# Kernel tuning notes

Measured on AMD Instinct MI355X. Metric: run time of the kernel, lower is better.

Reference implementation:

```python
import jax, jax.numpy as jnp
import numpy as np

G, N, F_IN, H, C = 128, 512, 128, 128, 10
LAMB = 1.0
NEG_SLOPE = 0.2
P_EDGE = 32.0 / N  # avg degree ~32


def setup_inputs() -> dict:
    key = jax.random.key(0)
    ks = jax.random.split(key, 12)
    x = jax.random.normal(ks[0], (G, N, F_IN), dtype=jnp.float32)
    # symmetric 0/1 adjacency without self loops (per-graph dense block)
    a = (jax.random.uniform(ks[1], (G, N, N)) < P_EDGE).astype(jnp.float32)
    adj = jnp.maximum(a, jnp.swapaxes(a, 1, 2)) * (1.0 - jnp.eye(N, dtype=jnp.float32))

    def lin(k, fi, fo):
        return (jax.random.normal(k, (fi, fo), dtype=jnp.float32) / np.float32(np.sqrt(fi)))

    return {
        "x": x, "adj": adj,
        "W1": lin(ks[2], F_IN, H), "b1": jnp.zeros((H,), jnp.float32),
        "W2": lin(ks[3], H, H), "b2": jnp.zeros((H,), jnp.float32),
        "W3": lin(ks[4], H, H), "b3": jnp.zeros((H,), jnp.float32),
        "att1_s": 0.1 * jax.random.normal(ks[5], (H,), dtype=jnp.float32),
        "att1_d": 0.1 * jax.random.normal(ks[6], (H,), dtype=jnp.float32),
        "att2_s": 0.1 * jax.random.normal(ks[7], (H,), dtype=jnp.float32),
        "att2_d": 0.1 * jax.random.normal(ks[8], (H,), dtype=jnp.float32),
        "Wl1": lin(ks[9], 2 * H, H), "bl1": jnp.zeros((H,), jnp.float32),
        "Wl2": lin(ks[10], H, H // 2), "bl2": jnp.zeros((H // 2,), jnp.float32),
        "Wl3": lin(ks[11], H // 2, C), "bl3": jnp.zeros((C,), jnp.float32),
    }


def gcn(x, adj, W, b):
    # GCNConv: D^{-1/2} (A + I) D^{-1/2} X W + b  (self-loop weight 1, edge weights in adj)
    deg = adj.sum(-1) + 1.0                              # [G, n]
    dinv = jax.lax.rsqrt(deg)
    xw = x @ W                                           # [G, n, H]
    agg = jnp.einsum('gij,gjf->gif', adj, dinv[..., None] * xw)
    return dinv[..., None] * agg + (dinv * dinv)[..., None] * xw + b


def info_score(x, adj):
    # HGP-SL node information score: row-wise L1 norm of (I - D^{-1} A) X
    deg = jnp.maximum(adj.sum(-1), 1.0)
    agg = jnp.einsum('gij,gjf->gif', adj, x) / deg[..., None]
    return jnp.sum(jnp.abs(x - agg), axis=-1)            # [G, n]


def hgpsl_pool(x, adj, att_s, att_d, k):
    # top-k node selection by information score, then structure learning:
    # dense (sample=False) path: e_ij = leaky_relu(att.[x_i||x_j]) + lamb*A_ij, softmax over j
    s = info_score(x, adj)
    _, idx = jax.lax.top_k(s, k)                         # [G, k]
    xk = jnp.take_along_axis(x, idx[..., None], axis=1)  # [G, k, H]
    g = jnp.arange(x.shape[0])[:, None, None]
    ak = adj[g, idx[:, :, None], idx[:, None, :]]        # induced adjacency [G, k, k]
    e = jax.nn.leaky_relu((xk @ att_s)[:, :, None] + (xk @ att_d)[:, None, :], NEG_SLOPE)
    attn = jax.nn.softmax(e + LAMB * ak, axis=-1)        # new learned edge weights
    return xk, attn


def readout(x):
    # gmp || gap over nodes
    return jnp.concatenate([x.max(axis=1), x.mean(axis=1)], axis=-1)


def reference(x, adj, W1, b1, W2, b2, W3, b3, att1_s, att1_d, att2_s, att2_d,
              Wl1, bl1, Wl2, bl2, Wl3, bl3):
    h = jax.nn.relu(gcn(x, adj, W1, b1))
    h, a1 = hgpsl_pool(h, adj, att1_s, att1_d, N // 2)
    x1 = readout(h)
    h = jax.nn.relu(gcn(h, a1, W2, b2))
    h, a2 = hgpsl_pool(h, a1, att2_s, att2_d, N // 4)
    x2 = readout(h)
    h = jax.nn.relu(gcn(h, a2, W3, b3))
    x3 = readout(h)
    z = jax.nn.relu(x1) + jax.nn.relu(x2) + jax.nn.relu(x3)
    z = jax.nn.relu(z @ Wl1 + bl1)
    z = jax.nn.relu(z @ Wl2 + bl2)
    return jax.nn.softmax(z @ Wl3 + bl3, axis=-1)
```

## Files before the change

kernel.cpp:

```cpp
#include <hip/hip_runtime.h>

#define Gg   128
#define N1   512
#define FH   128
#define K1   256
#define K2   128

typedef __bf16 bf16x8 __attribute__((ext_vector_type(8)));
typedef float  floatx4 __attribute__((ext_vector_type(4)));

__device__ inline float wredsum(float v) {
#pragma unroll
    for (int o = 32; o; o >>= 1) v += __shfl_xor(v, o, 64);
    return v;
}
__device__ inline float wredmax(float v) {
#pragma unroll
    for (int o = 32; o; o >>= 1) v = fmaxf(v, __shfl_xor(v, o, 64));
    return v;
}
__device__ inline unsigned short bf_rne(float x) {
    unsigned u = __float_as_uint(x);
    return (unsigned short)((u + 0x7fffu + ((u >> 16) & 1u)) >> 16);
}
__device__ __forceinline__ void gll16(const void* gsrc, void* lds) {
    __builtin_amdgcn_global_load_lds(
        (const __attribute__((address_space(1))) unsigned int*)gsrc,
        (__attribute__((address_space(3))) unsigned int*)lds, 16, 0, 0);
}

__global__ __launch_bounds__(256) void k_prep(const float* __restrict__ adj,
        unsigned short* __restrict__ adjbf,
        float* __restrict__ dinv_gcn, float* __restrict__ dinv_info) {
    int wave = threadIdx.x >> 6, lane = threadIdx.x & 63;
    long long row = (long long)blockIdx.x * 4 + wave;
    const float* ar = adj + row * N1;
    float s = 0.f;
    unsigned short ub[8] __attribute__((aligned(16)));
#pragma unroll
    for (int c = 0; c < 2; ++c) {
        float4 v = *(const float4*)(ar + lane * 8 + c * 4);
        s += (v.x + v.y) + (v.z + v.w);
        ub[c * 4 + 0] = (unsigned short)(__float_as_uint(v.x) >> 16);
        ub[c * 4 + 1] = (unsigned short)(__float_as_uint(v.y) >> 16);
        ub[c * 4 + 2] = (unsigned short)(__float_as_uint(v.z) >> 16);
        ub[c * 4 + 3] = (unsigned short)(__float_as_uint(v.w) >> 16);
    }
    *(uint4*)(adjbf + row * N1 + lane * 8) = *(const uint4*)ub;
    s = wredsum(s);
    if (lane == 0) {
        dinv_gcn[row]  = rsqrtf(s + 1.0f);
        dinv_info[row] = 1.0f / fmaxf(s, 1.0f);
    }
}

__global__ __launch_bounds__(256) void k_tsplit(const float* __restrict__ feat,
        unsigned short* __restrict__ Thi, unsigned short* __restrict__ Tmid,
        unsigned short* __restrict__ Tlo) {
    __shared__ float tile[64 * 65];
    int b = blockIdx.x;
    int g = b >> 4, rb = (b >> 1) & 7, cb = b & 1;
    int t = threadIdx.x;
    {
        int r0 = t >> 4, c4 = t & 15;
#pragma unroll
        for (int i = 0; i < 4; ++i) {
            int r = r0 + i * 16;
            float4 v = *(const float4*)(feat + ((long long)g * 512 + rb * 64 + r) * 128 + cb * 64 + c4 * 4);
            tile[r * 65 + c4 * 4 + 0] = v.x;
            tile[r * 65 + c4 * 4 + 1] = v.y;
            tile[r * 65 + c4 * 4 + 2] = v.z;
            tile[r * 65 + c4 * 4 + 3] = v.w;
        }
    }
    __syncthreads();
    int tf = t >> 2, chunk = t & 3;
    unsigned short hbuf[16] __attribute__((aligned(16)));
    unsigned short mbuf[16] __attribute__((aligned(16)));
    unsigned short lbuf[16] __attribute__((aligned(16)));
#pragma unroll
    for (int i = 0; i < 16; ++i) {
        int m = chunk * 16 + i;
        float v = tile[m * 65 + tf];
        unsigned short h = bf_rne(v);
        float fh = __uint_as_float((unsigned)h << 16);
        float r1 = v - fh;
        unsigned short md = bf_rne(r1);
        float fm = __uint_as_float((unsigned)md << 16);
        float r2 = r1 - fm;
        unsigned short lo = bf_rne(r2);
        hbuf[i] = h; mbuf[i] = md; lbuf[i] = lo;
    }
    int sxz = (tf >> 1) & 3;
    int c0 = (chunk & 1) * 2;
    int p0 = (c0 ^ sxz) * 8, p1 = ((c0 + 1) ^ sxz) * 8;
    long long obase = (long long)g * 65536 + (rb * 2 + (chunk >> 1)) * 4096
                    + (cb * 64 + tf) * 32;
    *(uint4*)(Thi + obase + p0)  = *(const uint4*)&hbuf[0];
    *(uint4*)(Thi + obase + p1)  = *(const uint4*)&hbuf[8];
    *(uint4*)(Tmid + obase + p0) = *(const uint4*)&mbuf[0];
    *(uint4*)(Tmid + obase + p1) = *(const uint4*)&mbuf[8];
    *(uint4*)(Tlo + obase + p0)  = *(const uint4*)&lbuf[0];
    *(uint4*)(Tlo + obase + p1)  = *(const uint4*)&lbuf[8];
}

template<int EPI>
__global__ __launch_bounds__(256) void k_aggmm(const unsigned short* __restrict__ adjbf,
        const unsigned short* __restrict__ Bhi, const unsigned short* __restrict__ Bmid,
        const unsigned short* __restrict__ Blo,
        const float* __restrict__ dvec, const float* __restrict__ hx,
        const float* __restrict__ bias, float* __restrict__ outH, float* __restrict__ outS) {
    __shared__ unsigned short Al[2][4096];
    __shared__ unsigned short Blin[2][3][4096];
    __shared__ float sred[2][128];
    int b = blockIdx.x;
    int g  = (b & 7) + ((b >> 5) << 3);
    int rb = (b >> 3) & 3;
    int tid = threadIdx.x;
    int w = tid >> 6, lane = tid & 63;
    int wm = w >> 1, wn = w & 1;
    int ln = lane & 15, quad = lane >> 4;
    int aoff = ((quad ^ ((lane >> 1) & 3)) << 4);
    floatx4 acc[4][4];
#pragma unroll
    for (int i = 0; i < 4; ++i)
#pragma unroll
        for (int j = 0; j < 4; ++j) { floatx4 z = {0.f, 0.f, 0.f, 0.f}; acc[i][j] = z; }

    const char* bsrc0 = (const char*)(Bhi  + (long long)g * 65536);
    const char* bsrc1 = (const char*)(Bmid + (long long)g * 65536);
    const char* bsrc2 = (const char*)(Blo  + (long long)g * 65536);
    int r1 = w * 32 + (lane >> 2);
    int c1 = (lane & 3) ^ ((r1 >> 1) & 3);
    int r2 = r1 + 16;
    int c2 = (lane & 3) ^ ((r2 >> 1) & 3);
    const unsigned short* abase = adjbf + ((long long)g * 512 + rb * 128) * 512;
    const unsigned short* asrc1 = abase + (long long)r1 * 512 + c1 * 8;
    const unsigned short* asrc2 = abase + (long long)r2 * 512 + c2 * 8;

#define STAGE(bi, kkv) do {                                                   \
        char* aldst = (char*)&Al[bi][0] + w * 2048;                           \
        gll16(asrc1 + (kkv), aldst);                                          \
        gll16(asrc2 + (kkv), aldst + 1024);                                   \
        long long soff = (long long)((kkv) >> 5) * 8192 + (w * 2048) + (lane << 4); \
        char* l0 = (char*)&Blin[bi][0][0] + w * 2048;                         \
        char* l1 = (char*)&Blin[bi][1][0] + w * 2048;                         \
        char* l2 = (char*)&Blin[bi][2][0] + w * 2048;                         \
        gll16(bsrc0 + soff,        l0);                                       \
        gll16(bsrc0 + soff + 1024, l0 + 1024);                                \
        gll16(bsrc1 + soff,        l1);                                       \
        gll16(bsrc1 + soff + 1024, l1 + 1024);                                \
        gll16(bsrc2 + soff,        l2);                                       \
        gll16(bsrc2 + soff + 1024, l2 + 1024);                                \
    } while (0)

    STAGE(0, 0);
    for (int kk = 0; kk < 512; kk += 32) {
        int cur = (kk >> 5) & 1;
        if (kk + 32 < 512) {
            STAGE(cur ^ 1, kk + 32);
            asm volatile("s_waitcnt vmcnt(8)" ::: "memory");
        } else {
            asm volatile("s_waitcnt vmcnt(0)" ::: "memory");
        }
        __builtin_amdgcn_sched_barrier(0);
        __builtin_amdgcn_s_barrier();
        bf16x8 af[4];
#pragma unroll
        for (int tm = 0; tm < 4; ++tm)
            af[tm] = *(const bf16x8*)((const char*)&Al[cur][0] + (wm * 64 + tm * 16 + ln) * 64 + aoff);
#pragma unroll
        for (int s = 0; s < 3; ++s) {
#pragma unroll
            for (int tn = 0; tn < 4; ++tn) {
                bf16x8 bfr = *(const bf16x8*)((const char*)&Blin[cur][s][0]
                                              + (wn * 64 + tn * 16 + ln) * 64 + aoff);
#pragma unroll
                for (int tm = 0; tm < 4; ++tm)
                    acc[tm][tn] = __builtin_amdgcn_mfma_f32_16x16x32_bf16(af[tm], bfr, acc[tm][tn], 0, 0, 0);
            }
        }
        __builtin_amdgcn_sched_barrier(0);
        __builtin_amdgcn_s_barrier();
    }
#undef STAGE
    long long rowbase = (long long)g * 512 + rb * 128;
    if (EPI == 0) {
#pragma unroll
        for (int tm = 0; tm < 4; ++tm)
#pragma unroll
        for (int r = 0; r < 4; ++r) {
            int ml = wm * 64 + tm * 16 + quad * 4 + r;
            long long grow = rowbase + ml;
            float di = dvec[grow];
#pragma unroll
            for (int tn = 0; tn < 4; ++tn) {
                int nc = wn * 64 + tn * 16 + ln;
                float hv = hx[grow * 128 + nc];
                float o = fmaxf(fmaf(di, acc[tm][tn][r] + hv, bias[nc]), 0.f);
                outH[grow * 128 + nc] = o;
            }
        }
    } else {
#pragma unroll
        for (int tm = 0; tm < 4; ++tm)
#pragma unroll
        for (int r = 0; r < 4; ++r) {
            int ml = wm * 64 + tm * 16 + quad * 4 + r;
            long long grow = rowbase + ml;
            float di = dvec[grow];
            float v = 0.f;
#pragma unroll
            for (int tn = 0; tn < 4; ++tn) {
                int nc = wn * 64 + tn * 16 + ln;
                float hv = hx[grow * 128 + nc];
                v += fabsf(hv - acc[tm][tn][r] * di);
            }
            v += __shfl_xor(v, 1); v += __shfl_xor(v, 2);
            v += __shfl_xor(v, 4); v += __shfl_xor(v, 8);
            if (ln == 0) sred[wn][ml] = v;
        }
        __syncthreads();
        if (tid < 128) outS[rowbase + tid] = sred[0][tid] + sred[1][tid];
    }
}

__global__ __launch_bounds__(256) void k_gemm_rw(const float* __restrict__ A,
        const float* __restrict__ W, float* __restrict__ C,
        const float* __restrict__ rs) {
    __shared__ float Al[64][68];
    __shared__ float Wl[64][132];
    long long row0 = (long long)blockIdx.x * 64;
    int tid = threadIdx.x, tr = tid >> 4, tc = tid & 15;
    float acc[4][8] = {};
    for (int ch = 0; ch < 2; ++ch) {
        for (int p = tid; p < 1024; p += 256) {
            int r = p >> 4, c4 = p & 15;
            *(float4*)&Al[r][c4 * 4] = *(const float4*)(A + (row0 + r) * 128 + ch * 64 + c4 * 4);
        }
        for (int p = tid; p < 2048; p += 256) {
            int r = p >> 5, c4 = p & 31;
            *(float4*)&Wl[r][c4 * 4] = *(const float4*)(W + (ch * 64 + r) * 128 + c4 * 4);
        }
        __syncthreads();
        for (int k = 0; k < 64; ++k) {
            float4 w0 = *(const float4*)&Wl[k][tc * 8];
            float4 w1 = *(const float4*)&Wl[k][tc * 8 + 4];
            float w[8] = {w0.x, w0.y, w0.z, w0.w, w1.x, w1.y, w1.z, w1.w};
#pragma unroll
            for (int i = 0; i < 4; ++i) {
                float a = Al[tr * 4 + i][k];
#pragma unroll
                for (int j = 0; j < 8; ++j) acc[i][j] = fmaf(a, w[j], acc[i][j]);
            }
        }
        __syncthreads();
    }
#pragma unroll
    for (int i = 0; i < 4; ++i) {
        long long r = row0 + tr * 4 + i;
        float sc = rs ? rs[r] : 1.0f;
        *(float4*)(C + r * 128 + tc * 8)     = make_float4(sc * acc[i][0], sc * acc[i][1], sc * acc[i][2], sc * acc[i][3]);
        *(float4*)(C + r * 128 + tc * 8 + 4) = make_float4(sc * acc[i][4], sc * acc[i][5], sc * acc[i][6], sc * acc[i][7]);
    }
}

template<int NT, int KSEL>
__global__ __launch_bounds__(256) void k_topk(const float* __restrict__ s, int* __restrict__ idx) {
    __shared__ unsigned long long keys[NT];
    int g = blockIdx.x;
    const float* sg = s + g * NT;
    for (int t = threadIdx.x; t < NT; t += 256) {
        unsigned int b = __float_as_uint(sg[t]);
        unsigned int ord = (b & 0x80000000u) ? ~b : (b | 0x80000000u);
        keys[t] = ((unsigned long long)(~ord) << 32) | (unsigned int)t;
    }
    __syncthreads();
    for (int k = 2; k <= NT; k <<= 1) {
        for (int j = k >> 1; j > 0; j >>= 1) {
            for (int i = threadIdx.x; i < NT; i += 256) {
                int l = i ^ j;
                if (l > i) {
                    bool dir = ((i & k) == 0);
                    unsigned long long a = keys[i], b2 = keys[l];
                    bool sw = dir ? (a > b2) : (a < b2);
                    if (sw) { keys[i] = b2; keys[l] = a; }
                }
            }
            __syncthreads();
        }
    }
    for (int t = threadIdx.x; t < KSEL; t += 256)
        idx[g * KSEL + t] = (int)(keys[t] & 0xffffffffu);
}

template<int KK>
__global__ __launch_bounds__(256) void k_gather(const float* __restrict__ h, int srcN,
        const int* __restrict__ idx, const float* __restrict__ atts, const float* __restrict__ attd,
        float* __restrict__ xk, float* __restrict__ as_, float* __restrict__ ad_) {
    int wave = threadIdx.x >> 6, lane = threadIdx.x & 63;
    int r = blockIdx.x * 4 + wave;
    int g = r / KK;
    int j = idx[r];
    float2 v = *(const float2*)(h + ((long long)g * srcN + j) * 128 + lane * 2);
    *(float2*)(xk + (long long)r * 128 + lane * 2) = v;
    float2 sv = *(const float2*)(atts + lane * 2);
    float2 dv = *(const float2*)(attd + lane * 2);
    float ps = v.x * sv.x + v.y * sv.y;
    float pd = v.x * dv.x + v.y * dv.y;
    ps = wredsum(ps); pd = wredsum(pd);
    if (lane == 0) { as_[r] = ps; ad_[r] = pd; }
}

template<int KK, int SRCN>
__global__ __launch_bounds__(256) void k_attn(const float* __restrict__ adjSrc,
        const int* __restrict__ idx, const float* __restrict__ as_, const float* __restrict__ ad_,
        float* __restrict__ attn, float* __restrict__ dgo, float* __restrict__ dio) {
    constexpr int E = KK / 64;
    __shared__ int   idxL[KK];
    __shared__ float adL[KK];
    __shared__ float rowL[4][SRCN];
    int bpg = KK / 4;
    int g = blockIdx.x / bpg;
    int wave = threadIdx.x >> 6, lane = threadIdx.x & 63;
    int i = (blockIdx.x % bpg) * 4 + wave;
    for (int t = threadIdx.x; t < KK; t += 256) { idxL[t] = idx[g * KK + t]; adL[t] = ad_[g * KK + t]; }
    __syncthreads();
    int ri = idxL[i];
    const float* arow = adjSrc + ((long long)g * SRCN + ri) * SRCN;
    for (int c = lane; c < SRCN; c += 64) rowL[wave][c] = arow[c];
    float asi = as_[g * KK + i];
    float vals[E];
    float m = -1e30f;
#pragma unroll
    for (int e = 0; e < E; ++e) {
        int j = e * 64 + lane;
        float x = asi + adL[j];
        x = (x >= 0.f) ? x : 0.2f * x;
        x += rowL[wave][idxL[j]];
        vals[e] = x; m = fmaxf(m, x);
    }
    m = wredmax(m);
    float S = 0.f;
#pragma unroll
    for (int e = 0; e < E; ++e) { vals[e] = expf(vals[e] - m); S += vals[e]; }
    S = wredsum(S);
    float inv = 1.f / S, rs = 0.f;
    float* orow = attn + ((long long)g * KK + i) * KK;
#pragma unroll
    for (int e = 0; e < E; ++e) { float p = vals[e] * inv; rs += p; orow[e * 64 + lane] = p; }
    rs = wredsum(rs);
    if (lane == 0) { dgo[g * KK + i] = rsqrtf(rs + 1.f); dio[g * KK + i] = 1.f / fmaxf(rs, 1.f); }
}

template<int KK>
__global__ __launch_bounds__(128) void k_readout(const float* __restrict__ xk, float* __restrict__ xo) {
    int g = blockIdx.x, f = threadIdx.x;
    const float* p = xk + (long long)g * KK * 128 + f;
    float m = -1e30f, s = 0.f;
    for (int r = 0; r < KK; ++r) { float v = p[r * 128]; m = fmaxf(m, v); s += v; }
    xo[g * 256 + f] = m;
    xo[g * 256 + 128 + f] = s * (1.0f / KK);
}

template<int KK, bool SCALEY, int EPI>
__global__ __launch_bounds__(256) void k_agg(const float* __restrict__ A, const float* __restrict__ Y,
        const float* __restrict__ dg, const float* __restrict__ di_,
        const float* __restrict__ bias, const float* __restrict__ hx,
        float* __restrict__ outH, float* __restrict__ outS) {
    __shared__ float Al[64][68];
    __shared__ float Yl[64][132];
    __shared__ float red[64][17];
    constexpr int RB = KK / 64;
    int g = blockIdx.x / RB;
    int rb = blockIdx.x % RB;
    const float* Ag = A + (long long)g * KK * KK;
    const float* Yg = Y + (long long)g * KK * 128;
    int tid = threadIdx.x, tr = tid >> 4, tc = tid & 15;
    float acc[4][8] = {};
    for (int ch = 0; ch < KK / 64; ++ch) {
        for (int p = tid; p < 1024; p += 256) {
            int r = p >> 4, c4 = p & 15;
            *(float4*)&Al[r][c4 * 4] = *(const float4*)(Ag + (rb * 64 + r) * KK + ch * 64 + c4 * 4);
        }
        for (int p = tid; p < 2048; p += 256) {
            int r = p >> 5, c4 = p & 31;
            float4 v = *(const float4*)(Yg + (ch * 64 + r) * 128 + c4 * 4);
            if (SCALEY) { float sc = dg[g * KK + ch * 64 + r]; v.x *= sc; v.y *= sc; v.z *= sc; v.w *= sc; }
            *(float4*)&Yl[r][c4 * 4] = v;
        }
        __syncthreads();
        for (int k = 0; k < 64; ++k) {
            float4 w0 = *(const float4*)&Yl[k][tc * 8];
            float4 w1 = *(const float4*)&Yl[k][tc * 8 + 4];
            float w[8] = {w0.x, w0.y, w0.z, w0.w, w1.x, w1.y, w1.z, w1.w};
#pragma unroll
            for (int i = 0; i < 4; ++i) {
                float a = Al[tr * 4 + i][k];
#pragma unroll
                for (int j = 0; j < 8; ++j) acc[i][j] = fmaf(a, w[j], acc[i][j]);
            }
        }
        __syncthreads();
    }
    int i0 = rb * 64 + tr * 4;
    if (EPI == 0) {
#pragma unroll
        for (int i = 0; i < 4; ++i) {
            long long gi = (long long)g * KK + i0 + i;
            float d = dg[gi], dd = d * d;
            float4 x0 = *(const float4*)(hx + gi * 128 + tc * 8);
            float4 x1 = *(const float4*)(hx + gi * 128 + tc * 8 + 4);
            float4 b0 = *(const float4*)(bias + tc * 8);
            float4 b1 = *(const float4*)(bias + tc * 8 + 4);
            float4 o0, o1;
            o0.x = fmaxf(fmaf(d, acc[i][0], fmaf(dd, x0.x, b0.x)), 0.f);
            o0.y = fmaxf(fmaf(d, acc[i][1], fmaf(dd, x0.y, b0.y)), 0.f);
            o0.z = fmaxf(fmaf(d, acc[i][2], fmaf(dd, x0.z, b0.z)), 0.f);
            o0.w = fmaxf(fmaf(d, acc[i][3], fmaf(dd, x0.w, b0.w)), 0.f);
            o1.x = fmaxf(fmaf(d, acc[i][4], fmaf(dd, x1.x, b1.x)), 0.f);
            o1.y = fmaxf(fmaf(d, acc[i][5], fmaf(dd, x1.y, b1.y)), 0.f);
            o1.z = fmaxf(fmaf(d, acc[i][6], fmaf(dd, x1.z, b1.z)), 0.f);
            o1.w = fmaxf(fmaf(d, acc[i][7], fmaf(dd, x1.w, b1.w)), 0.f);
            *(float4*)(outH + gi * 128 + tc * 8)     = o0;
            *(float4*)(outH + gi * 128 + tc * 8 + 4) = o1;
        }
    } else {
#pragma unroll
        for (int i = 0; i < 4; ++i) {
            long long gi = (long long)g * KK + i0 + i;
            float d = di_[gi];
            float4 x0 = *(const float4*)(hx + gi * 128 + tc * 8);
            float4 x1 = *(const float4*)(hx + gi * 128 + tc * 8 + 4);
            float p = fabsf(x0.x - acc[i][0] * d) + fabsf(x0.y - acc[i][1] * d)
                    + fabsf(x0.z - acc[i][2] * d) + fabsf(x0.w - acc[i][3] * d)
                    + fabsf(x1.x - acc[i][4] * d) + fabsf(x1.y - acc[i][5] * d)
                    + fabsf(x1.z - acc[i][6] * d) + fabsf(x1.w - acc[i][7] * d);
            red[tr * 4 + i][tc] = p;
        }
        __syncthreads();
        if (tid < 64) {
            float s = 0.f;
#pragma unroll
            for (int t = 0; t < 16; ++t) s += red[tid][t];
            outS[(long long)g * KK + rb * 64 + tid] = s;
        }
    }
}

__global__ __launch_bounds__(128) void k_mlp(const float* __restrict__ x1, const float* __restrict__ x2,
        const float* __restrict__ x3,
        const float* __restrict__ Wl1, const float* __restrict__ bl1,
        const float* __restrict__ Wl2, const float* __restrict__ bl2,
        const float* __restrict__ Wl3, const float* __restrict__ bl3,
        float* __restrict__ out) {
    __shared__ float z[256], z1[128], z2[64], lg[10];
    int g = blockIdx.x, t = threadIdx.x;
    for (int k = t; k < 256; k += 128)
        z[k] = fmaxf(x1[g * 256 + k], 0.f) + fmaxf(x2[g * 256 + k], 0.f) + fmaxf(x3[g * 256 + k], 0.f);
    __syncthreads();
    {
        float acc = bl1[t];
        for (int k = 0; k < 256; ++k) acc = fmaf(z[k], Wl1[k * 128 + t], acc);
        z1[t] = fmaxf(acc, 0.f);
    }
    __syncthreads();
    if (t < 64) {
        float acc = bl2[t];
        for (int k = 0; k < 128; ++k) acc = fmaf(z1[k], Wl2[k * 64 + t], acc);
        z2[t] = fmaxf(acc, 0.f);
    }
    __syncthreads();
    if (t < 10) {
        float acc = bl3[t];
        for (int k = 0; k < 64; ++k) acc = fmaf(z2[k], Wl3[k * 10 + t], acc);
        lg[t] = acc;
    }
    __syncthreads();
    if (t == 0) {
        float m = -1e30f;
        for (int c = 0; c < 10; ++c) m = fmaxf(m, lg[c]);
        float S = 0.f;
        float e[10];
        for (int c = 0; c < 10; ++c) { e[c] = expf(lg[c] - m); S += e[c]; }
        float inv = 1.f / S;
        for (int c = 0; c < 10; ++c) out[g * 10 + c] = e[c] * inv;
    }
}

extern "C" void kernel_launch(void* const* d_in, const int* in_sizes, int n_in,
                              void* d_out, int out_size, void* d_ws, size_t ws_size,
                              hipStream_t stream) {
    const float* x     = (const float*)d_in[0];
    const float* adj   = (const float*)d_in[1];
    const float* W1    = (const float*)d_in[2];
    const float* b1    = (const float*)d_in[3];
    const float* W2    = (const float*)d_in[4];
    const float* b2    = (const float*)d_in[5];
    const float* W3    = (const float*)d_in[6];
    const float* b3    = (const float*)d_in[7];
    const float* att1s = (const float*)d_in[8];
    const float* att1d = (const float*)d_in[9];
    const float* att2s = (const float*)d_in[10];
    const float* att2d = (const float*)d_in[11];
    const float* Wl1   = (const float*)d_in[12];
    const float* bl1   = (const float*)d_in[13];
    const float* Wl2   = (const float*)d_in[14];
    const float* bl2   = (const float*)d_in[15];
    const float* Wl3   = (const float*)d_in[16];
    const float* bl3   = (const float*)d_in[17];
    float* out = (float*)d_out;

    char* ws = (char*)d_ws;
    unsigned short* Thi  = (unsigned short*)(ws + 0);
    unsigned short* Tmid = (unsigned short*)(ws + 16777216);
    unsigned short* Tlo  = (unsigned short*)(ws + 33554432);
    float* xk1 = (float*)(ws + 0);
    float* xw2 = (float*)(ws + 16777216);
    float* h2  = (float*)(ws + 33554432);
    float* xk2 = (float*)(ws + 16777216);
    float* a2  = (float*)(ws + 25165824);
    float* xw3 = (float*)(ws + 0);
    float* h3  = (float*)(ws + 8388608);
    float* dxw1 = (float*)(ws + 50331648);
    float* h1   = dxw1;
    float* a1   = dxw1;
    float* s1      = (float*)(ws + 83886080);
    int*   idx1    = (int*)  (ws + 84148224);
    float* as1     = (float*)(ws + 84279296);
    float* ad1     = (float*)(ws + 84410368);
    float* dinv_g1 = (float*)(ws + 84541440);
    float* dinv_i1 = (float*)(ws + 84803584);
    float* dinv_g2 = (float*)(ws + 85065728);
    float* dinv_i2 = (float*)(ws + 85196800);
    float* x1r     = (float*)(ws + 85327872);
    float* s2      = (float*)(ws + 85458944);
    int*   idx2    = (int*)  (ws + 85590016);
    float* as2     = (float*)(ws + 85655552);
    float* ad2     = (float*)(ws + 85721088);
    float* dinv_g3 = (float*)(ws + 85786624);
    float* dinv_i3 = (float*)(ws + 85852160);
    float* x2r     = (float*)(ws + 85917696);
    float* x3r     = (float*)(ws + 86048768);
    unsigned short* adjbf = (unsigned short*)(ws + 100663296);

    k_prep<<<Gg * N1 / 4, 256, 0, stream>>>(adj, adjbf, dinv_g1, dinv_i1);
    k_gemm_rw<<<Gg * N1 / 64, 256, 0, stream>>>(x, W1, dxw1, dinv_g1);
    k_tsplit<<<Gg * 16, 256, 0, stream>>>(dxw1, Thi, Tmid, Tlo);
    k_aggmm<0><<<Gg * 4, 256, 0, stream>>>(adjbf, Thi, Tmid, Tlo, dinv_g1, dxw1, b1, h1, nullptr);
    k_tsplit<<<Gg * 16, 256, 0, stream>>>(h1, Thi, Tmid, Tlo);
    k_aggmm<1><<<Gg * 4, 256, 0, stream>>>(adjbf, Thi, Tmid, Tlo, dinv_i1, h1, nullptr, nullptr, s1);
    k_topk<N1, K1><<<Gg, 256, 0, stream>>>(s1, idx1);
    k_gather<K1><<<Gg * K1 / 4, 256, 0, stream>>>(h1, N1, idx1, att1s, att1d, xk1, as1, ad1);
    k_readout<K1><<<Gg, 128, 0, stream>>>(xk1, x1r);
    k_attn<K1, N1><<<Gg * K1 / 4, 256, 0, stream>>>(adj, idx1, as1, ad1, a1, dinv_g2, dinv_i2);

    k_gemm_rw<<<Gg * K1 / 64, 256, 0, stream>>>(xk1, W2, xw2, nullptr);
    k_agg<K1, true, 0><<<Gg * (K1 / 64), 256, 0, stream>>>(a1, xw2, dinv_g2, dinv_i2, b2, xw2, h2, nullptr);
    k_agg<K1, false, 1><<<Gg * (K1 / 64), 256, 0, stream>>>(a1, h2, dinv_g2, dinv_i2, b2, h2, nullptr, s2);
    k_topk<K1, K2><<<Gg, 256, 0, stream>>>(s2, idx2);
    k_gather<K2><<<Gg * K2 / 4, 256, 0, stream>>>(h2, K1, idx2, att2s, att2d, xk2, as2, ad2);
    k_readout<K2><<<Gg, 128, 0, stream>>>(xk2, x2r);
    k_attn<K2, K1><<<Gg * K2 / 4, 256, 0, stream>>>(a1, idx2, as2, ad2, a2, dinv_g3, dinv_i3);

    k_gemm_rw<<<Gg * K2 / 64, 256, 0, stream>>>(xk2, W3, xw3, nullptr);
    k_agg<K2, true, 0><<<Gg * (K2 / 64), 256, 0, stream>>>(a2, xw3, dinv_g3, dinv_i3, b3, xw3, h3, nullptr);
    k_readout<K2><<<Gg, 128, 0, stream>>>(h3, x3r);

    k_mlp<<<Gg, 128, 0, stream>>>(x1r, x2r, x3r, Wl1, bl1, Wl2, bl2, Wl3, bl3, out);
}
```

Baseline: 608.3 us.

## Fuse prep with first GEMM, readouts into attention and MLP, bf16 adjacency rows

Merges the adjacency prep kernel and the first feature GEMM into one launch with disjoint block ranges. The dinv row scaling moves into the split kernel and the epilogue. The readout kernels are folded into the attention kernels as extra blocks, and the final readout into the MLP kernel. The first attention kernel now reads the bf16 adjacency instead of fp32. Together these cut launch count and adjacency read bandwidth, at the cost of a simpler non-MFMA fp32 GEMM path and an unoptimised serial readout in the MLP.

Measured after the change: 580.4 us (median of 2 runs). 4.6% less time.

```diff
diff --git a/kernel.cpp b/kernel.cpp
--- a/kernel.cpp
+++ b/kernel.cpp
@@ -29,32 +29,71 @@
         (__attribute__((address_space(3))) unsigned int*)lds, 16, 0, 0);
 }
 
-__global__ __launch_bounds__(256) void k_prep(const float* __restrict__ adj,
+__global__ __launch_bounds__(256) void k_prep_gemm(const float* __restrict__ adj,
         unsigned short* __restrict__ adjbf,
-        float* __restrict__ dinv_gcn, float* __restrict__ dinv_info) {
-    int wave = threadIdx.x >> 6, lane = threadIdx.x & 63;
-    long long row = (long long)blockIdx.x * 4 + wave;
-    const float* ar = adj + row * N1;
-    float s = 0.f;
-    unsigned short ub[8] __attribute__((aligned(16)));
-#pragma unroll
-    for (int c = 0; c < 2; ++c) {
-        float4 v = *(const float4*)(ar + lane * 8 + c * 4);
-        s += (v.x + v.y) + (v.z + v.w);
-        ub[c * 4 + 0] = (unsigned short)(__float_as_uint(v.x) >> 16);
-        ub[c * 4 + 1] = (unsigned short)(__float_as_uint(v.y) >> 16);
-        ub[c * 4 + 2] = (unsigned short)(__float_as_uint(v.z) >> 16);
-        ub[c * 4 + 3] = (unsigned short)(__float_as_uint(v.w) >> 16);
-    }
-    *(uint4*)(adjbf + row * N1 + lane * 8) = *(const uint4*)ub;
-    s = wredsum(s);
-    if (lane == 0) {
-        dinv_gcn[row]  = rsqrtf(s + 1.0f);
-        dinv_info[row] = 1.0f / fmaxf(s, 1.0f);
+        float* __restrict__ dinv_gcn, float* __restrict__ dinv_info,
+        const float* __restrict__ A, const float* __restrict__ W, float* __restrict__ C) {
+    __shared__ float Al[64][68];
+    __shared__ float Wl[64][132];
+    if (blockIdx.x < Gg * N1 / 64) {
+        long long row0 = (long long)blockIdx.x * 64;
+        int tid = threadIdx.x, tr = tid >> 4, tc = tid & 15;
+        float acc[4][8] = {};
+        for (int ch = 0; ch < 2; ++ch) {
+            for (int p = tid; p < 1024; p += 256) {
+                int r = p >> 4, c4 = p & 15;
+                *(float4*)&Al[r][c4 * 4] = *(const float4*)(A + (row0 + r) * 128 + ch * 64 + c4 * 4);
+            }
+            for (int p = tid; p < 2048; p += 256) {
+                int r = p >> 5, c4 = p & 31;
+                *(float4*)&Wl[r][c4 * 4] = *(const float4*)(W + (ch * 64 + r) * 128 + c4 * 4);
+            }
+            __syncthreads();
+            for (int k = 0; k < 64; ++k) {
+                float4 w0 = *(const float4*)&Wl[k][tc * 8];
+                float4 w1 = *(const float4*)&Wl[k][tc * 8 + 4];
+                float w[8] = {w0.x, w0.y, w0.z, w0.w, w1.x, w1.y, w1.z, w1.w};
+#pragma unroll
+                for (int i = 0; i < 4; ++i) {
+                    float a = Al[tr * 4 + i][k];
+#pragma unroll
+                    for (int j = 0; j < 8; ++j) acc[i][j] = fmaf(a, w[j], acc[i][j]);
+                }
+            }
+            __syncthreads();
+        }
+#pragma unroll
+        for (int i = 0; i < 4; ++i) {
+            long long r = row0 + tr * 4 + i;
+            *(float4*)(C + r * 128 + tc * 8)     = make_float4(acc[i][0], acc[i][1], acc[i][2], acc[i][3]);
+            *(float4*)(C + r * 128 + tc * 8 + 4) = make_float4(acc[i][4], acc[i][5], acc[i][6], acc[i][7]);
+        }
+    } else {
+        int wave = threadIdx.x >> 6, lane = threadIdx.x & 63;
+        long long row = (long long)(blockIdx.x - Gg * N1 / 64) * 4 + wave;
+        const float* ar = adj + row * N1;
+        float s = 0.f;
+        unsigned short ub[8] __attribute__((aligned(16)));
+#pragma unroll
+        for (int c = 0; c < 2; ++c) {
+            float4 v = *(const float4*)(ar + lane * 8 + c * 4);
+            s += (v.x + v.y) + (v.z + v.w);
+            ub[c * 4 + 0] = (unsigned short)(__float_as_uint(v.x) >> 16);
+            ub[c * 4 + 1] = (unsigned short)(__float_as_uint(v.y) >> 16);
+            ub[c * 4 + 2] = (unsigned short)(__float_as_uint(v.z) >> 16);
+            ub[c * 4 + 3] = (unsigned short)(__float_as_uint(v.w) >> 16);
+        }
+        *(uint4*)(adjbf + row * N1 + lane * 8) = *(const uint4*)ub;
+        s = wredsum(s);
+        if (lane == 0) {
+            dinv_gcn[row]  = rsqrtf(s + 1.0f);
+            dinv_info[row] = 1.0f / fmaxf(s, 1.0f);
+        }
     }
 }
 
 __global__ __launch_bounds__(256) void k_tsplit(const float* __restrict__ feat,
+        const float* __restrict__ rs,
         unsigned short* __restrict__ Thi, unsigned short* __restrict__ Tmid,
         unsigned short* __restrict__ Tlo) {
     __shared__ float tile[64 * 65];
@@ -67,6 +106,10 @@
         for (int i = 0; i < 4; ++i) {
             int r = r0 + i * 16;
             float4 v = *(const float4*)(feat + ((long long)g * 512 + rb * 64 + r) * 128 + cb * 64 + c4 * 4);
+            if (rs) {
+                float sc = rs[(long long)g * 512 + rb * 64 + r];
+                v.x *= sc; v.y *= sc; v.z *= sc; v.w *= sc;
+            }
             tile[r * 65 + c4 * 4 + 0] = v.x;
             tile[r * 65 + c4 * 4 + 1] = v.y;
             tile[r * 65 + c4 * 4 + 2] = v.z;
@@ -197,7 +240,7 @@
             for (int tn = 0; tn < 4; ++tn) {
                 int nc = wn * 64 + tn * 16 + ln;
                 float hv = hx[grow * 128 + nc];
-                float o = fmaxf(fmaf(di, acc[tm][tn][r] + hv, bias[nc]), 0.f);
+                float o = fmaxf(fmaf(di, acc[tm][tn][r] + di * hv, bias[nc]), 0.f);
                 outH[grow * 128 + nc] = o;
             }
         }
@@ -312,14 +355,27 @@
     if (lane == 0) { as_[r] = ps; ad_[r] = pd; }
 }
 
-template<int KK, int SRCN>
-__global__ __launch_bounds__(256) void k_attn(const float* __restrict__ adjSrc,
+template<int KK, int SRCN, bool BF16>
+__global__ __launch_bounds__(256) void k_attnro(const void* __restrict__ adjSrc,
         const int* __restrict__ idx, const float* __restrict__ as_, const float* __restrict__ ad_,
-        float* __restrict__ attn, float* __restrict__ dgo, float* __restrict__ dio) {
+        float* __restrict__ attn, float* __restrict__ dgo, float* __restrict__ dio,
+        const float* __restrict__ xk, float* __restrict__ xo) {
     constexpr int E = KK / 64;
+    constexpr int nAttn = Gg * KK / 4;
     __shared__ int   idxL[KK];
     __shared__ float adL[KK];
     __shared__ float rowL[4][SRCN];
+    if ((int)blockIdx.x >= nAttn) {
+        int g = blockIdx.x - nAttn, t = threadIdx.x;
+        if (t < 128) {
+            const float* p = xk + (long long)g * KK * 128 + t;
+            float m = -1e30f, s = 0.f;
+            for (int r = 0; r < KK; ++r) { float v = p[r * 128]; m = fmaxf(m, v); s += v; }
+            xo[g * 256 + t] = m;
+            xo[g * 256 + 128 + t] = s * (1.0f / KK);
+        }
+        return;
+    }
     int bpg = KK / 4;
     int g = blockIdx.x / bpg;
     int wave = threadIdx.x >> 6, lane = threadIdx.x & 63;
@@ -327,8 +383,14 @@
     for (int t = threadIdx.x; t < KK; t += 256) { idxL[t] = idx[g * KK + t]; adL[t] = ad_[g * KK + t]; }
     __syncthreads();
     int ri = idxL[i];
-    const float* arow = adjSrc + ((long long)g * SRCN + ri) * SRCN;
-    for (int c = lane; c < SRCN; c += 64) rowL[wave][c] = arow[c];
+    if (BF16) {
+        const unsigned short* arow = (const unsigned short*)adjSrc + ((long long)g * SRCN + ri) * SRCN;
+        for (int c = lane; c < SRCN; c += 64)
+            rowL[wave][c] = __uint_as_float((unsigned)arow[c] << 16);
+    } else {
+        const float* arow = (const float*)adjSrc + ((long long)g * SRCN + ri) * SRCN;
+        for (int c = lane; c < SRCN; c += 64) rowL[wave][c] = arow[c];
+    }
     float asi = as_[g * KK + i];
     float vals[E];
     float m = -1e30f;
@@ -351,16 +413,6 @@
     for (int e = 0; e < E; ++e) { float p = vals[e] * inv; rs += p; orow[e * 64 + lane] = p; }
     rs = wredsum(rs);
     if (lane == 0) { dgo[g * KK + i] = rsqrtf(rs + 1.f); dio[g * KK + i] = 1.f / fmaxf(rs, 1.f); }
-}
-
-template<int KK>
-__global__ __launch_bounds__(128) void k_readout(const float* __restrict__ xk, float* __restrict__ xo) {
-    int g = blockIdx.x, f = threadIdx.x;
-    const float* p = xk + (long long)g * KK * 128 + f;
-    float m = -1e30f, s = 0.f;
-    for (int r = 0; r < KK; ++r) { float v = p[r * 128]; m = fmaxf(m, v); s += v; }
-    xo[g * 256 + f] = m;
-    xo[g * 256 + 128 + f] = s * (1.0f / KK);
 }
 
 template<int KK, bool SCALEY, int EPI>
@@ -449,15 +501,21 @@
 }
 
 __global__ __launch_bounds__(128) void k_mlp(const float* __restrict__ x1, const float* __restrict__ x2,
-        const float* __restrict__ x3,
+        const float* __restrict__ h3,
         const float* __restrict__ Wl1, const float* __restrict__ bl1,
         const float* __restrict__ Wl2, const float* __restrict__ bl2,
         const float* __restrict__ Wl3, const float* __restrict__ bl3,
         float* __restrict__ out) {
     __shared__ float z[256], z1[128], z2[64], lg[10];
     int g = blockIdx.x, t = threadIdx.x;
-    for (int k = t; k < 256; k += 128)
-        z[k] = fmaxf(x1[g * 256 + k], 0.f) + fmaxf(x2[g * 256 + k], 0.f) + fmaxf(x3[g * 256 + k], 0.f);
+    {
+        const float* p = h3 + (long long)g * K2 * 128 + t;
+        float m = -1e30f, s = 0.f;
+        for (int r = 0; r < K2; ++r) { float v = p[r * 128]; m = fmaxf(m, v); s += v; }
+        float x3a = m, x3b = s * (1.0f / K2);
+        z[t]       = fmaxf(x1[g * 256 + t], 0.f)       + fmaxf(x2[g * 256 + t], 0.f)       + fmaxf(x3a, 0.f);
+        z[t + 128] = fmaxf(x1[g * 256 + 128 + t], 0.f) + fmaxf(x2[g * 256 + 128 + t], 0.f) + fmaxf(x3b, 0.f);
+    }
     __syncthreads();
     {
         float acc = bl1[t];
@@ -541,31 +599,26 @@
     float* dinv_g3 = (float*)(ws + 85786624);
     float* dinv_i3 = (float*)(ws + 85852160);
     float* x2r     = (float*)(ws + 85917696);
-    float* x3r     = (float*)(ws + 86048768);
     unsigned short* adjbf = (unsigned short*)(ws + 100663296);
 
-    k_prep<<<Gg * N1 / 4, 256, 0, stream>>>(adj, adjbf, dinv_g1, dinv_i1);
-    k_gemm_rw<<<Gg * N1 / 64, 256, 0, stream>>>(x, W1, dxw1, dinv_g1);
-    k_tsplit<<<Gg * 16, 256, 0, stream>>>(dxw1, Thi, Tmid, Tlo);
+    k_prep_gemm<<<Gg * N1 / 64 + Gg * N1 / 4, 256, 0, stream>>>(adj, adjbf, dinv_g1, dinv_i1, x, W1, dxw1);
+    k_tsplit<<<Gg * 16, 256, 0, stream>>>(dxw1, dinv_g1, Thi, Tmid, Tlo);
     k_aggmm<0><<<Gg * 4, 256, 0, stream>>>(adjbf, Thi, Tmid, Tlo, dinv_g1, dxw1, b1, h1, nullptr);
-    k_tsplit<<<Gg * 16, 256, 0, stream>>>(h1, Thi, Tmid, Tlo);
+    k_tsplit<<<Gg * 16, 256, 0, stream>>>(h1, nullptr, Thi, Tmid, Tlo);
     k_aggmm<1><<<Gg * 4, 256, 0, stream>>>(adjbf, Thi, Tmid, Tlo, dinv_i1, h1, nullptr, nullptr, s1);
     k_topk<N1, K1><<<Gg, 256, 0, stream>>>(s1, idx1);
     k_gather<K1><<<Gg * K1 / 4, 256, 0, stream>>>(h1, N1, idx1, att1s, att1d, xk1, as1, ad1);
-    k_readout<K1><<<Gg, 128, 0, stream>>>(xk1, x1r);
-    k_attn<K1, N1><<<Gg * K1 / 4, 256, 0, stream>>>(adj, idx1, as1, ad1, a1, dinv_g2, dinv_i2);
+    k_attnro<K1, N1, true><<<Gg * K1 / 4 + Gg, 256, 0, stream>>>(adjbf, idx1, as1, ad1, a1, dinv_g2, dinv_i2, xk1, x1r);
 
     k_gemm_rw<<<Gg * K1 / 64, 256, 0, stream>>>(xk1, W2, xw2, nullptr);
     k_agg<K1, true, 0><<<Gg * (K1 / 64), 256, 0, stream>>>(a1, xw2, dinv_g2, dinv_i2, b2, xw2, h2, nullptr);
     k_agg<K1, false, 1><<<Gg * (K1 / 64), 256, 0, stream>>>(a1, h2, dinv_g2, dinv_i2, b2, h2, nullptr, s2);
     k_topk<K1, K2><<<Gg, 256, 0, stream>>>(s2, idx2);
     k_gather<K2><<<Gg * K2 / 4, 256, 0, stream>>>(h2, K1, idx2, att2s, att2d, xk2, as2, ad2);
-    k_readout<K2><<<Gg, 128, 0, stream>>>(xk2, x2r);
-    k_attn<K2, K1><<<Gg * K2 / 4, 256, 0, stream>>>(a1, idx2, as2, ad2, a2, dinv_g3, dinv_i3);
+    k_attnro<K2, K1, false><<<Gg * K2 / 4 + Gg, 256, 0, stream>>>(a1, idx2, as2, ad2, a2, dinv_g3, dinv_i3, xk2, x2r);
 
     k_gemm_rw<<<Gg * K2 / 64, 256, 0, stream>>>(xk2, W3, xw3, nullptr);
     k_agg<K2, true, 0><<<Gg * (K2 / 64), 256, 0, stream>>>(a2, xw3, dinv_g3, dinv_i3, b3, xw3, h3, nullptr);
-    k_readout<K2><<<Gg, 128, 0, stream>>>(h3, x3r);
-
-    k_mlp<<<Gg, 128, 0, stream>>>(x1r, x2r, x3r, Wl1, bl1, Wl2, bl2, Wl3, bl3, out);
-}
+
+    k_mlp<<<Gg, 128, 0, stream>>>(x1r, x2r, h3, Wl1, bl1, Wl2, bl2, Wl3, bl3, out);
+}
```
